# Optimization experiments

Hardware: AMD Instinct MI355X
Metric: run time of the kernel (lower is better)

Reference implementation:

```python
import jax, jax.numpy as jnp
import numpy as np

B, H, L, D = 4, 16, 2048, 128


def setup_inputs() -> dict:
    key = jax.random.key(0)
    kx, kw1, kb1, kw2, kb2 = jax.random.split(key, 5)
    s = 1.0 / np.sqrt(D)
    return {
        "x": jax.random.normal(kx, (B, H, L, D), dtype=jnp.float32),
        "W1": jax.random.uniform(kw1, (D, D), jnp.float32, -s, s),
        "b1": jax.random.uniform(kb1, (D,), jnp.float32, -s, s),
        "W2": jax.random.uniform(kw2, (D, D), jnp.float32, -s, s),
        "b2": jax.random.uniform(kb2, (D,), jnp.float32, -s, s),
    }


def reference(x, W1, b1, W2, b2):
    # proj_1/proj_2: Linear(dim, dim) on the last axis (torch stores W as [out,in])
    q = jnp.einsum('bhld,ed->bhle', x, W1) + b1  # [B,H,L,D]
    k = jnp.einsum('bhld,ed->bhle', x, W2) + b2  # [B,H,L,D]
    # exact-erf GELU on raw QK^T scores, then softmax over j
    adj = jax.nn.gelu(jnp.einsum('bhid,bhjd->bhij', q, k), approximate=False)
    adj = jax.nn.softmax(adj, axis=-1)  # [B,H,L,L]
    # dropout is identity in eval mode
    out = jnp.einsum('bhij,bhjd->bhid', adj, x)  # [B,H,L,D]
    return out.transpose(0, 2, 1, 3).reshape(B, L, H * D)
```

## Files before the change

kernel.cpp:

```cpp
#include <hip/hip_runtime.h>
#include <hip/hip_bf16.h>

#define B_ 4
#define H_ 16
#define L_ 2048
#define D_ 128
#define BH_ 64

typedef __attribute__((ext_vector_type(8))) _Float16 f16x8;
typedef __attribute__((ext_vector_type(4))) float f32x4;
typedef __attribute__((ext_vector_type(16))) float f32x16;
typedef __attribute__((ext_vector_type(2))) unsigned u32x2;

#define L2E 1.44269504088896f

__device__ __forceinline__ float gelu_m(float v, float negm) {
  float u  = v * v;
  float m1 = 0.044715f * u;
  float w  = __builtin_fmaf(m1, v, v);
  float e  = __builtin_amdgcn_exp2f(-2.3020575f * w);
  float r  = __builtin_amdgcn_rcpf(1.0f + e);
  float t  = 1.44269504f * v;
  return __builtin_fmaf(t, r, negm);
}

__device__ __forceinline__ void gl2lds16(const void* g, void* l) {
  __builtin_amdgcn_global_load_lds(
      (const __attribute__((address_space(1))) void*)g,
      (__attribute__((address_space(3))) void*)l, 16, 0, 0);
}

__device__ __forceinline__ unsigned pkrtz(float a, float b) {
  auto t = __builtin_amdgcn_cvt_pkrtz(a, b);
  return __builtin_bit_cast(unsigned, t);
}

__global__ __launch_bounds__(256) void wcvt_kernel(
    const float* __restrict__ W1, const float* __restrict__ W2,
    _Float16* __restrict__ Wh1, _Float16* __restrict__ Wh2)
{
  int i = blockIdx.x * 256 + threadIdx.x;
  Wh1[i] = (_Float16)W1[i];
  Wh2[i] = (_Float16)W2[i];
}

__global__ __launch_bounds__(256) void proj_tr_kernel(
    const float* __restrict__ x,
    const _Float16* __restrict__ Wh1, const float* __restrict__ b1,
    const _Float16* __restrict__ Wh2, const float* __restrict__ b2,
    _Float16* __restrict__ Qb, _Float16* __restrict__ Kb,
    _Float16* __restrict__ VT)
{
  const int tid  = threadIdx.x;
  const int wave = tid >> 6;
  const int lane = tid & 63;
  const int lhi  = lane >> 4;
  const int llo  = lane & 15;
  const int r0   = blockIdx.x * 64;
  const int wr0  = r0 + wave * 16;

  f16x8 a[4];
#pragma unroll
  for (int ks = 0; ks < 4; ++ks) {
    const f32x4* p = (const f32x4*)(x + (size_t)(wr0 + llo) * D_ + lhi * 8 + ks * 32);
    f32x4 f0 = p[0], f1 = p[1];
    union { unsigned u[4]; f16x8 v; } t;
    t.u[0] = pkrtz(f0[0], f0[1]);
    t.u[1] = pkrtz(f0[2], f0[3]);
    t.u[2] = pkrtz(f1[0], f1[1]);
    t.u[3] = pkrtz(f1[2], f1[3]);
    a[ks] = t.v;
  }

  f32x4 accq[8], acck[8];
#pragma unroll
  for (int n = 0; n < 8; ++n) {
    accq[n] = (f32x4){0.f, 0.f, 0.f, 0.f};
    acck[n] = (f32x4){0.f, 0.f, 0.f, 0.f};
  }

#pragma unroll
  for (int n = 0; n < 8; ++n) {
    const int e = n * 16 + llo;
#pragma unroll
    for (int ks = 0; ks < 4; ++ks) {
      f16x8 w1f = *(const f16x8*)(Wh1 + (size_t)e * D_ + lhi * 8 + ks * 32);
      f16x8 w2f = *(const f16x8*)(Wh2 + (size_t)e * D_ + lhi * 8 + ks * 32);
      accq[n] = __builtin_amdgcn_mfma_f32_16x16x32_f16(a[ks], w1f, accq[n], 0, 0, 0);
      acck[n] = __builtin_amdgcn_mfma_f32_16x16x32_f16(a[ks], w2f, acck[n], 0, 0, 0);
    }
  }

#pragma unroll
  for (int n = 0; n < 8; ++n) {
    const int e = n * 16 + llo;
    const float bias1 = b1[e];
    const float bias2 = b2[e];
#pragma unroll
    for (int r = 0; r < 4; ++r) {
      const size_t row = (size_t)wr0 + lhi * 4 + r;
      Qb[row * D_ + e] = (_Float16)(accq[n][r] + bias1);
      Kb[row * D_ + e] = (_Float16)(acck[n][r] + bias2);
    }
  }

  const int bh = r0 / L_;
  const int l0 = r0 % L_;
  const int d  = tid & 127;
  const int rh = tid >> 7;
  _Float16* dst = VT + (size_t)bh * D_ * L_ + (size_t)d * L_ + l0 + rh * 32;
#pragma unroll
  for (int j = 0; j < 4; ++j) {
    union { unsigned u[4]; f16x8 v; } t;
#pragma unroll
    for (int e = 0; e < 4; ++e) {
      float x0 = x[(size_t)(r0 + rh * 32 + j * 8 + 2 * e)     * D_ + d];
      float x1 = x[(size_t)(r0 + rh * 32 + j * 8 + 2 * e + 1) * D_ + d];
      t.u[e] = pkrtz(x0, x1);
    }
    *(f16x8*)(dst + j * 8) = t.v;
  }
}

__global__ __launch_bounds__(512) void attn_kernel(
    const _Float16* __restrict__ Qb, const _Float16* __restrict__ Kb,
    const _Float16* __restrict__ VT, float* __restrict__ out)
{
  __shared__ _Float16 Ks[2][128 * 128];
  __shared__ _Float16 Vs[2][128 * 128];

  const int tid  = threadIdx.x;
  const int wave = tid >> 6;
  const int lane = tid & 63;
  const int l5   = lane & 31;
  const int hi   = lane >> 5;

  const int bid = blockIdx.x;
  const int blk = (bid & 7) * 64 + (bid >> 3);
  const int bh  = blk >> 3;
  const int q0  = (blk & 7) * 256;
  const int b   = bh >> 4;
  const int h   = bh & 15;
  const int wq0 = q0 + wave * 32;

  const char* KheadB = (const char*)(Kb + (size_t)bh * L_ * D_);
  const char* VheadB = (const char*)(VT + (size_t)bh * D_ * L_);

  int sdst[4], ksrc[4], vsrc[4];
#pragma unroll
  for (int c = 0; c < 4; ++c) {
    const int row = c * 32 + wave * 4 + (lane >> 4);
    const int c0  = (lane & 15) * 8;
    sdst[c] = c * 8192 + wave * 1024;
    ksrc[c] = row * 256  + 2 * (c0 ^ ((row & 15) << 3));
    vsrc[c] = row * 4096 + 2 * (c0 ^ ((row & 15) << 3));
  }
  const int swz4 = (l5 & 15) << 3;

  f16x8 qf[8];
#pragma unroll
  for (int s = 0; s < 8; ++s)
    qf[s] = *(const f16x8*)(Qb + ((size_t)bh * L_ + wq0 + l5) * D_ + s * 16 + hi * 8);

  f32x16 accO[4];
#pragma unroll
  for (int n = 0; n < 4; ++n)
#pragma unroll
    for (int r = 0; r < 16; ++r) accO[n][r] = 0.f;
  float negm = 64.f;
  float l = 0.f;

#pragma unroll
  for (int c = 0; c < 4; ++c) {
    gl2lds16(KheadB + ksrc[c], (char*)&Ks[0][0] + sdst[c]);
    gl2lds16(VheadB + vsrc[c], (char*)&Vs[0][0] + sdst[c]);
  }
  __syncthreads();

  for (int ts = 0; ts < L_ / 128; ++ts) {
    const int cur = ts & 1;
    if (ts + 1 < L_ / 128) {
      const char* kt_ = KheadB + (size_t)(ts + 1) * 32768;
      const char* vt_ = VheadB + (size_t)(ts + 1) * 256;
#pragma unroll
      for (int c = 0; c < 4; ++c) {
        gl2lds16(kt_ + ksrc[c], (char*)&Ks[cur ^ 1][0] + sdst[c]);
        gl2lds16(vt_ + vsrc[c], (char*)&Vs[cur ^ 1][0] + sdst[c]);
      }
    }
    const _Float16* Vcur = &Vs[cur][0];

#pragma unroll
    for (int half = 0; half < 2; ++half) {
      const _Float16* Kcur = &Ks[cur][half * 64 * 128];
      const int vt0 = half * 64;

      f32x16 sA, sB;
#pragma unroll
      for (int r = 0; r < 16; ++r) { sA[r] = 0.f; sB[r] = 0.f; }
      __builtin_amdgcn_s_setprio(1);
#pragma unroll
      for (int s = 0; s < 8; ++s) {
        f16x8 kfa = *(const f16x8*)(Kcur + l5 * 128 +
                                    ((s * 16 + hi * 8) ^ swz4));
        sA = __builtin_amdgcn_mfma_f32_32x32x16_f16(kfa, qf[s], sA, 0, 0, 0);
        f16x8 kfb = *(const f16x8*)(Kcur + (32 + l5) * 128 +
                                    ((s * 16 + hi * 8) ^ swz4));
        sB = __builtin_amdgcn_mfma_f32_32x32x16_f16(kfb, qf[s], sB, 0, 0, 0);
      }
      __builtin_amdgcn_s_setprio(0);

      auto softmax_pv = [&](const f32x16& sT, int vkbase) {
        float gm[16];
#pragma unroll
        for (int r = 0; r < 16; ++r) gm[r] = gelu_m(sT[r], negm);

        float p[16];
#pragma unroll
        for (int r = 0; r < 16; ++r) p[r] = __builtin_amdgcn_exp2f(gm[r]);

        float tm = fmaxf(fmaxf(gm[0], gm[1]), gm[2]);
        tm = fmaxf(fmaxf(tm, gm[3]),  gm[4]);
        tm = fmaxf(fmaxf(tm, gm[5]),  gm[6]);
        tm = fmaxf(fmaxf(tm, gm[7]),  gm[8]);
        tm = fmaxf(fmaxf(tm, gm[9]),  gm[10]);
        tm = fmaxf(fmaxf(tm, gm[11]), gm[12]);
        tm = fmaxf(fmaxf(tm, gm[13]), gm[14]);
        tm = fmaxf(tm, gm[15]);
        tm = fmaxf(tm, __shfl_xor(tm, 32));

        if (!__all(tm <= 11.5415603f)) {
          float dm = fmaxf(tm, 0.f);
          negm -= dm;
          float sc = __builtin_amdgcn_exp2f(-dm);
#pragma unroll
          for (int r = 0; r < 16; ++r) p[r] *= sc;
          l *= sc;
          float scr[16];
#pragma unroll
          for (int r = 0; r < 16; ++r)
            scr[r] = __shfl(sc, (r & 3) + 8 * (r >> 2) + 4 * hi);
#pragma unroll
          for (int n = 0; n < 4; ++n)
#pragma unroll
            for (int r = 0; r < 16; ++r) accO[n][r] *= scr[r];
        }

        float a0 = p[0]+p[1],   a1 = p[2]+p[3],   a2 = p[4]+p[5],   a3 = p[6]+p[7];
        float a4 = p[8]+p[9],   a5 = p[10]+p[11], a6 = p[12]+p[13], a7 = p[14]+p[15];
        l += ((a0+a1)+(a2+a3)) + ((a4+a5)+(a6+a7));

        unsigned pk01 = pkrtz(p[0], p[1]),   pk23 = pkrtz(p[2], p[3]);
        unsigned pk45 = pkrtz(p[4], p[5]),   pk67 = pkrtz(p[6], p[7]);
        unsigned pk89 = pkrtz(p[8], p[9]),   pkAB = pkrtz(p[10], p[11]);
        unsigned pkCD = pkrtz(p[12], p[13]), pkEF = pkrtz(p[14], p[15]);
        u32x2 r0 = __builtin_amdgcn_permlane32_swap(pk01, pk45, false, false);
        u32x2 r1 = __builtin_amdgcn_permlane32_swap(pk23, pk67, false, false);
        u32x2 r2 = __builtin_amdgcn_permlane32_swap(pk89, pkCD, false, false);
        u32x2 r3 = __builtin_amdgcn_permlane32_swap(pkAB, pkEF, false, false);
        union { unsigned u[4]; f16x8 v; } A0c, A1c;
        A0c.u[0] = r0[0]; A0c.u[1] = r1[0]; A0c.u[2] = r0[1]; A0c.u[3] = r1[1];
        A1c.u[0] = r2[0]; A1c.u[1] = r3[0]; A1c.u[2] = r2[1]; A1c.u[3] = r3[1];

        __builtin_amdgcn_s_setprio(1);
#pragma unroll
        for (int n = 0; n < 4; ++n) {
          f16x8 vf0 = *(const f16x8*)(Vcur + (n * 32 + l5) * 128 +
                                      ((vkbase + hi * 8) ^ swz4));
          accO[n] = __builtin_amdgcn_mfma_f32_32x32x16_f16(A0c.v, vf0, accO[n], 0, 0, 0);
          f16x8 vf1 = *(const f16x8*)(Vcur + (n * 32 + l5) * 128 +
                                      ((vkbase + 16 + hi * 8) ^ swz4));
          accO[n] = __builtin_amdgcn_mfma_f32_32x32x16_f16(A1c.v, vf1, accO[n], 0, 0, 0);
        }
        __builtin_amdgcn_s_setprio(0);
      };

      softmax_pv(sA, vt0);
      softmax_pv(sB, vt0 + 32);
    }

    __syncthreads();
  }

  l += __shfl_xor(l, 32);
  float linv = __builtin_amdgcn_rcpf(l);
  float lb[16];
#pragma unroll
  for (int r = 0; r < 16; ++r)
    lb[r] = __shfl(linv, (r & 3) + 8 * (r >> 2) + 4 * hi);
#pragma unroll
  for (int n = 0; n < 4; ++n)
#pragma unroll
    for (int r = 0; r < 16; ++r) {
      const int i = wq0 + (r & 3) + 8 * (r >> 2) + 4 * hi;
      out[((size_t)(b * L_ + i) * H_ + h) * D_ + n * 32 + l5] = accO[n][r] * lb[r];
    }
}

extern "C" void kernel_launch(void* const* d_in, const int* in_sizes, int n_in,
                              void* d_out, int out_size, void* d_ws, size_t ws_size,
                              hipStream_t stream) {
  const float* x  = (const float*)d_in[0];
  const float* W1 = (const float*)d_in[1];
  const float* b1 = (const float*)d_in[2];
  const float* W2 = (const float*)d_in[3];
  const float* b2 = (const float*)d_in[4];
  float* out = (float*)d_out;

  const size_t N = (size_t)BH_ * L_ * D_;
  _Float16* Qb = (_Float16*)d_ws;
  _Float16* Kb = Qb + N;
  _Float16* VT = Kb + N;

  _Float16* Wh1 = (_Float16*)d_out;
  _Float16* Wh2 = Wh1 + D_ * D_;

  wcvt_kernel<<<64, 256, 0, stream>>>(W1, W2, Wh1, Wh2);
  proj_tr_kernel<<<(BH_ * L_) / 64, 256, 0, stream>>>(x, Wh1, b1, Wh2, b2, Qb, Kb, VT);
  attn_kernel<<<BH_ * (L_ / 256), 512, 0, stream>>>(Qb, Kb, VT, out);
}
```

Baseline: 328.4 us.

## Shrink attention blocks to 128 queries and 64-key tiles

The attention kernel now runs 256-thread blocks (4 waves, 128 query rows) instead of 512-thread blocks, and streams K/V in 64-key tiles instead of 128-key tiles. LDS use per block drops from 128KB to 64KB, so more blocks can be resident per CU, and the grid doubles to 1024 blocks. The staging index maps and the V swizzle change to fit the narrower V tile. The cost is half as much K/V reuse per block, so more global and L2 traffic, and twice as many barriers per key sweep.

Measured after the change: 441.6 us. 34.5% more time.

```diff
diff --git a/kernel.cpp b/kernel.cpp
--- a/kernel.cpp
+++ b/kernel.cpp
@@ -122,12 +122,12 @@
   }
 }
 
-__global__ __launch_bounds__(512) void attn_kernel(
+__global__ __launch_bounds__(256) void attn_kernel(
     const _Float16* __restrict__ Qb, const _Float16* __restrict__ Kb,
     const _Float16* __restrict__ VT, float* __restrict__ out)
 {
-  __shared__ _Float16 Ks[2][128 * 128];
-  __shared__ _Float16 Vs[2][128 * 128];
+  __shared__ _Float16 Ks[2][64 * 128];
+  __shared__ _Float16 Vs[2][128 * 64];
 
   const int tid  = threadIdx.x;
   const int wave = tid >> 6;
@@ -136,9 +136,9 @@
   const int hi   = lane >> 5;
 
   const int bid = blockIdx.x;
-  const int blk = (bid & 7) * 64 + (bid >> 3);
-  const int bh  = blk >> 3;
-  const int q0  = (blk & 7) * 256;
+  const int blk = (bid & 7) * 128 + (bid >> 3);
+  const int bh  = blk >> 4;
+  const int q0  = (blk & 15) * 128;
   const int b   = bh >> 4;
   const int h   = bh & 15;
   const int wq0 = q0 + wave * 32;
@@ -146,16 +146,24 @@
   const char* KheadB = (const char*)(Kb + (size_t)bh * L_ * D_);
   const char* VheadB = (const char*)(VT + (size_t)bh * D_ * L_);
 
-  int sdst[4], ksrc[4], vsrc[4];
+  int kdst[4], ksrc[4], vdst[4], vsrc[4];
 #pragma unroll
   for (int c = 0; c < 4; ++c) {
-    const int row = c * 32 + wave * 4 + (lane >> 4);
-    const int c0  = (lane & 15) * 8;
-    sdst[c] = c * 8192 + wave * 1024;
-    ksrc[c] = row * 256  + 2 * (c0 ^ ((row & 15) << 3));
-    vsrc[c] = row * 4096 + 2 * (c0 ^ ((row & 15) << 3));
-  }
-  const int swz4 = (l5 & 15) << 3;
+    {
+      const int krow = c * 16 + wave * 4 + (lane >> 4);
+      const int c0   = (lane & 15) * 8;
+      kdst[c] = c * 4096 + wave * 1024;
+      ksrc[c] = krow * 256 + 2 * (c0 ^ ((krow & 15) << 3));
+    }
+    {
+      const int vrow = c * 32 + wave * 8 + (lane >> 3);
+      const int c0   = (lane & 7) * 8;
+      vdst[c] = c * 4096 + wave * 1024;
+      vsrc[c] = vrow * 4096 + 2 * (c0 ^ ((vrow & 7) << 3));
+    }
+  }
+  const int swzK = (l5 & 15) << 3;
+  const int swzV = (l5 & 7) << 3;
 
   f16x8 qf[8];
 #pragma unroll
@@ -172,112 +180,107 @@
 
 #pragma unroll
   for (int c = 0; c < 4; ++c) {
-    gl2lds16(KheadB + ksrc[c], (char*)&Ks[0][0] + sdst[c]);
-    gl2lds16(VheadB + vsrc[c], (char*)&Vs[0][0] + sdst[c]);
+    gl2lds16(KheadB + ksrc[c], (char*)&Ks[0][0] + kdst[c]);
+    gl2lds16(VheadB + vsrc[c], (char*)&Vs[0][0] + vdst[c]);
   }
   __syncthreads();
 
-  for (int ts = 0; ts < L_ / 128; ++ts) {
-    const int cur = ts & 1;
-    if (ts + 1 < L_ / 128) {
-      const char* kt_ = KheadB + (size_t)(ts + 1) * 32768;
-      const char* vt_ = VheadB + (size_t)(ts + 1) * 256;
+  for (int t = 0; t < L_ / 64; ++t) {
+    const int cur = t & 1;
+    if (t + 1 < L_ / 64) {
+      const char* kt_ = KheadB + (size_t)(t + 1) * 16384;
+      const char* vt_ = VheadB + (size_t)(t + 1) * 128;
 #pragma unroll
       for (int c = 0; c < 4; ++c) {
-        gl2lds16(kt_ + ksrc[c], (char*)&Ks[cur ^ 1][0] + sdst[c]);
-        gl2lds16(vt_ + vsrc[c], (char*)&Vs[cur ^ 1][0] + sdst[c]);
+        gl2lds16(kt_ + ksrc[c], (char*)&Ks[cur ^ 1][0] + kdst[c]);
+        gl2lds16(vt_ + vsrc[c], (char*)&Vs[cur ^ 1][0] + vdst[c]);
       }
     }
+    const _Float16* Kcur = &Ks[cur][0];
     const _Float16* Vcur = &Vs[cur][0];
 
-#pragma unroll
-    for (int half = 0; half < 2; ++half) {
-      const _Float16* Kcur = &Ks[cur][half * 64 * 128];
-      const int vt0 = half * 64;
-
-      f32x16 sA, sB;
-#pragma unroll
-      for (int r = 0; r < 16; ++r) { sA[r] = 0.f; sB[r] = 0.f; }
+    f32x16 sA, sB;
+#pragma unroll
+    for (int r = 0; r < 16; ++r) { sA[r] = 0.f; sB[r] = 0.f; }
+    __builtin_amdgcn_s_setprio(1);
+#pragma unroll
+    for (int s = 0; s < 8; ++s) {
+      f16x8 kfa = *(const f16x8*)(Kcur + l5 * 128 +
+                                  ((s * 16 + hi * 8) ^ swzK));
+      sA = __builtin_amdgcn_mfma_f32_32x32x16_f16(kfa, qf[s], sA, 0, 0, 0);
+      f16x8 kfb = *(const f16x8*)(Kcur + (32 + l5) * 128 +
+                                  ((s * 16 + hi * 8) ^ swzK));
+      sB = __builtin_amdgcn_mfma_f32_32x32x16_f16(kfb, qf[s], sB, 0, 0, 0);
+    }
+    __builtin_amdgcn_s_setprio(0);
+
+    auto softmax_pv = [&](const f32x16& sT, int vkbase) {
+      float gm[16];
+#pragma unroll
+      for (int r = 0; r < 16; ++r) gm[r] = gelu_m(sT[r], negm);
+
+      float p[16];
+#pragma unroll
+      for (int r = 0; r < 16; ++r) p[r] = __builtin_amdgcn_exp2f(gm[r]);
+
+      float tm = fmaxf(fmaxf(gm[0], gm[1]), gm[2]);
+      tm = fmaxf(fmaxf(tm, gm[3]),  gm[4]);
+      tm = fmaxf(fmaxf(tm, gm[5]),  gm[6]);
+      tm = fmaxf(fmaxf(tm, gm[7]),  gm[8]);
+      tm = fmaxf(fmaxf(tm, gm[9]),  gm[10]);
+      tm = fmaxf(fmaxf(tm, gm[11]), gm[12]);
+      tm = fmaxf(fmaxf(tm, gm[13]), gm[14]);
+      tm = fmaxf(tm, gm[15]);
+      tm = fmaxf(tm, __shfl_xor(tm, 32));
+
+      if (!__all(tm <= 11.5415603f)) {
+        float dm = fmaxf(tm, 0.f);
+        negm -= dm;
+        float sc = __builtin_amdgcn_exp2f(-dm);
+#pragma unroll
+        for (int r = 0; r < 16; ++r) p[r] *= sc;
+        l *= sc;
+        float scr[16];
+#pragma unroll
+        for (int r = 0; r < 16; ++r)
+          scr[r] = __shfl(sc, (r & 3) + 8 * (r >> 2) + 4 * hi);
+#pragma unroll
+        for (int n = 0; n < 4; ++n)
+#pragma unroll
+          for (int r = 0; r < 16; ++r) accO[n][r] *= scr[r];
+      }
+
+      float a0 = p[0]+p[1],   a1 = p[2]+p[3],   a2 = p[4]+p[5],   a3 = p[6]+p[7];
+      float a4 = p[8]+p[9],   a5 = p[10]+p[11], a6 = p[12]+p[13], a7 = p[14]+p[15];
+      l += ((a0+a1)+(a2+a3)) + ((a4+a5)+(a6+a7));
+
+      unsigned pk01 = pkrtz(p[0], p[1]),   pk23 = pkrtz(p[2], p[3]);
+      unsigned pk45 = pkrtz(p[4], p[5]),   pk67 = pkrtz(p[6], p[7]);
+      unsigned pk89 = pkrtz(p[8], p[9]),   pkAB = pkrtz(p[10], p[11]);
+      unsigned pkCD = pkrtz(p[12], p[13]), pkEF = pkrtz(p[14], p[15]);
+      u32x2 r0 = __builtin_amdgcn_permlane32_swap(pk01, pk45, false, false);
+      u32x2 r1 = __builtin_amdgcn_permlane32_swap(pk23, pk67, false, false);
+      u32x2 r2 = __builtin_amdgcn_permlane32_swap(pk89, pkCD, false, false);
+      u32x2 r3 = __builtin_amdgcn_permlane32_swap(pkAB, pkEF, false, false);
+      union { unsigned u[4]; f16x8 v; } A0c, A1c;
+      A0c.u[0] = r0[0]; A0c.u[1] = r1[0]; A0c.u[2] = r0[1]; A0c.u[3] = r1[1];
+      A1c.u[0] = r2[0]; A1c.u[1] = r3[0]; A1c.u[2] = r2[1]; A1c.u[3] = r3[1];
+
       __builtin_amdgcn_s_setprio(1);
 #pragma unroll
-      for (int s = 0; s < 8; ++s) {
-        f16x8 kfa = *(const f16x8*)(Kcur + l5 * 128 +
-                                    ((s * 16 + hi * 8) ^ swz4));
-        sA = __builtin_amdgcn_mfma_f32_32x32x16_f16(kfa, qf[s], sA, 0, 0, 0);
-        f16x8 kfb = *(const f16x8*)(Kcur + (32 + l5) * 128 +
-                                    ((s * 16 + hi * 8) ^ swz4));
-        sB = __builtin_amdgcn_mfma_f32_32x32x16_f16(kfb, qf[s], sB, 0, 0, 0);
+      for (int n = 0; n < 4; ++n) {
+        f16x8 vf0 = *(const f16x8*)(Vcur + (n * 32 + l5) * 64 +
+                                    ((vkbase + hi * 8) ^ swzV));
+        accO[n] = __builtin_amdgcn_mfma_f32_32x32x16_f16(A0c.v, vf0, accO[n], 0, 0, 0);
+        f16x8 vf1 = *(const f16x8*)(Vcur + (n * 32 + l5) * 64 +
+                                    ((vkbase + 16 + hi * 8) ^ swzV));
+        accO[n] = __builtin_amdgcn_mfma_f32_32x32x16_f16(A1c.v, vf1, accO[n], 0, 0, 0);
       }
       __builtin_amdgcn_s_setprio(0);
-
-      auto softmax_pv = [&](const f32x16& sT, int vkbase) {
-        float gm[16];
-#pragma unroll
-        for (int r = 0; r < 16; ++r) gm[r] = gelu_m(sT[r], negm);
-
-        float p[16];
-#pragma unroll
-        for (int r = 0; r < 16; ++r) p[r] = __builtin_amdgcn_exp2f(gm[r]);
-
-        float tm = fmaxf(fmaxf(gm[0], gm[1]), gm[2]);
-        tm = fmaxf(fmaxf(tm, gm[3]),  gm[4]);
-        tm = fmaxf(fmaxf(tm, gm[5]),  gm[6]);
-        tm = fmaxf(fmaxf(tm, gm[7]),  gm[8]);
-        tm = fmaxf(fmaxf(tm, gm[9]),  gm[10]);
-        tm = fmaxf(fmaxf(tm, gm[11]), gm[12]);
-        tm = fmaxf(fmaxf(tm, gm[13]), gm[14]);
-        tm = fmaxf(tm, gm[15]);
-        tm = fmaxf(tm, __shfl_xor(tm, 32));
-
-        if (!__all(tm <= 11.5415603f)) {
-          float dm = fmaxf(tm, 0.f);
-          negm -= dm;
-          float sc = __builtin_amdgcn_exp2f(-dm);
-#pragma unroll
-          for (int r = 0; r < 16; ++r) p[r] *= sc;
-          l *= sc;
-          float scr[16];
-#pragma unroll
-          for (int r = 0; r < 16; ++r)
-            scr[r] = __shfl(sc, (r & 3) + 8 * (r >> 2) + 4 * hi);
-#pragma unroll
-          for (int n = 0; n < 4; ++n)
-#pragma unroll
-            for (int r = 0; r < 16; ++r) accO[n][r] *= scr[r];
-        }
-
-        float a0 = p[0]+p[1],   a1 = p[2]+p[3],   a2 = p[4]+p[5],   a3 = p[6]+p[7];
-        float a4 = p[8]+p[9],   a5 = p[10]+p[11], a6 = p[12]+p[13], a7 = p[14]+p[15];
-        l += ((a0+a1)+(a2+a3)) + ((a4+a5)+(a6+a7));
-
-        unsigned pk01 = pkrtz(p[0], p[1]),   pk23 = pkrtz(p[2], p[3]);
-        unsigned pk45 = pkrtz(p[4], p[5]),   pk67 = pkrtz(p[6], p[7]);
-        unsigned pk89 = pkrtz(p[8], p[9]),   pkAB = pkrtz(p[10], p[11]);
-        unsigned pkCD = pkrtz(p[12], p[13]), pkEF = pkrtz(p[14], p[15]);
-        u32x2 r0 = __builtin_amdgcn_permlane32_swap(pk01, pk45, false, false);
-        u32x2 r1 = __builtin_amdgcn_permlane32_swap(pk23, pk67, false, false);
-        u32x2 r2 = __builtin_amdgcn_permlane32_swap(pk89, pkCD, false, false);
-        u32x2 r3 = __builtin_amdgcn_permlane32_swap(pkAB, pkEF, false, false);
-        union { unsigned u[4]; f16x8 v; } A0c, A1c;
-        A0c.u[0] = r0[0]; A0c.u[1] = r1[0]; A0c.u[2] = r0[1]; A0c.u[3] = r1[1];
-        A1c.u[0] = r2[0]; A1c.u[1] = r3[0]; A1c.u[2] = r2[1]; A1c.u[3] = r3[1];
-
-        __builtin_amdgcn_s_setprio(1);
-#pragma unroll
-        for (int n = 0; n < 4; ++n) {
-          f16x8 vf0 = *(const f16x8*)(Vcur + (n * 32 + l5) * 128 +
-                                      ((vkbase + hi * 8) ^ swz4));
-          accO[n] = __builtin_amdgcn_mfma_f32_32x32x16_f16(A0c.v, vf0, accO[n], 0, 0, 0);
-          f16x8 vf1 = *(const f16x8*)(Vcur + (n * 32 + l5) * 128 +
-                                      ((vkbase + 16 + hi * 8) ^ swz4));
-          accO[n] = __builtin_amdgcn_mfma_f32_32x32x16_f16(A1c.v, vf1, accO[n], 0, 0, 0);
-        }
-        __builtin_amdgcn_s_setprio(0);
-      };
-
-      softmax_pv(sA, vt0);
-      softmax_pv(sB, vt0 + 32);
-    }
+    };
+
+    softmax_pv(sA, 0);
+    softmax_pv(sB, 32);
 
     __syncthreads();
   }
@@ -317,5 +320,5 @@
 
   wcvt_kernel<<<64, 256, 0, stream>>>(W1, W2, Wh1, Wh2);
   proj_tr_kernel<<<(BH_ * L_) / 64, 256, 0, stream>>>(x, Wh1, b1, Wh2, b2, Qb, Kb, VT);
-  attn_kernel<<<BH_ * (L_ / 256), 512, 0, stream>>>(Qb, Kb, VT, out);
-}
+  attn_kernel<<<BH_ * (L_ / 128), 256, 0, stream>>>(Qb, Kb, VT, out);
+}
```
